# Kernel tuning notes

Measured on AMD Instinct MI355X. Metric: run time of the kernel, lower is better.

## Reference

```python
import jax, jax.numpy as jnp
import numpy as np


def setup_inputs() -> dict:
    key = jax.random.key(0)
    ks = jax.random.split(key, 8)
    T, D = 8192, 36
    return {
        "embeddings": jax.random.normal(ks[0], (T, D), dtype=jnp.float32),
        "WQ_prog": jax.random.normal(ks[1], (2, D), dtype=jnp.float32),
        "WK_prog": jax.random.normal(ks[2], (2, D), dtype=jnp.float32),
        "WV_op": jax.random.normal(ks[3], (1, D), dtype=jnp.float32),
        "WV_arg": jax.random.normal(ks[4], (1, D), dtype=jnp.float32),
        "WQ_stack": jax.random.normal(ks[5], (2, D), dtype=jnp.float32),
        "WK_stack": jax.random.normal(ks[6], (2, D), dtype=jnp.float32),
        "WV_stack": jax.random.normal(ks[7], (1, D), dtype=jnp.float32),
    }


def reference(embeddings, WQ_prog, WK_prog, WV_op, WV_arg, WQ_stack, WK_stack, WV_stack):
    # --- program-fetch head: hard-argmax attention ---
    Q_prog = embeddings @ WQ_prog.T          # (T, 2)
    K_prog = embeddings @ WK_prog.T          # (T, 2)
    V_op = embeddings @ WV_op.T              # (T, 1)
    V_arg = embeddings @ WV_arg.T            # (T, 1)
    scores_prog = Q_prog @ K_prog.T          # (T, T)
    best_prog = jnp.argmax(scores_prog, axis=1)   # (T,)
    fetched_ops = V_op[best_prog, 0]
    fetched_args = V_arg[best_prog, 0]

    # --- stack-fetch head: hard-argmax attention ---
    Q_stack = embeddings @ WQ_stack.T        # (T, 2)
    K_stack = embeddings @ WK_stack.T        # (T, 2)
    V_stack = embeddings @ WV_stack.T        # (T, 1)
    scores_stack = Q_stack @ K_stack.T       # (T, T)
    best_stack = jnp.argmax(scores_stack, axis=1)
    fetched_vals = V_stack[best_stack, 0]

    return (fetched_ops, fetched_args, fetched_vals)
```

## Files before the change

kernel.cpp:

```cpp
#include <hip/hip_runtime.h>
#include <math.h>

#define T 8192
#define D 36
#define NCH 8
#define CHUNK (T / NCH)


__global__ __launch_bounds__(256) void proj_kernel(
    const float* __restrict__ E,
    const float* __restrict__ WQp, const float* __restrict__ WKp,
    const float* __restrict__ WVop, const float* __restrict__ WVarg,
    const float* __restrict__ WQs, const float* __restrict__ WKs,
    const float* __restrict__ WVs, float* __restrict__ ws) {
    int t = blockIdx.x * blockDim.x + threadIdx.x;
    if (t >= T) return;
    float e[D];
    const float4* Er = (const float4*)(E + t * D);
#pragma unroll
    for (int i = 0; i < D / 4; ++i) {
        float4 v = Er[i];
        e[4 * i + 0] = v.x; e[4 * i + 1] = v.y;
        e[4 * i + 2] = v.z; e[4 * i + 3] = v.w;
    }
    float qp0 = 0.f, qp1 = 0.f, kp0 = 0.f, kp1 = 0.f;
    float qs0 = 0.f, qs1 = 0.f, ks0 = 0.f, ks1 = 0.f;
    float vop = 0.f, varg = 0.f, vs = 0.f;
#pragma unroll
    for (int d = 0; d < D; ++d) {
        float ed = e[d];
        qp0 = fmaf(ed, WQp[d], qp0);
        qp1 = fmaf(ed, WQp[D + d], qp1);
        kp0 = fmaf(ed, WKp[d], kp0);
        kp1 = fmaf(ed, WKp[D + d], kp1);
        qs0 = fmaf(ed, WQs[d], qs0);
        qs1 = fmaf(ed, WQs[D + d], qs1);
        ks0 = fmaf(ed, WKs[d], ks0);
        ks1 = fmaf(ed, WKs[D + d], ks1);
        vop  = fmaf(ed, WVop[d], vop);
        varg = fmaf(ed, WVarg[d], varg);
        vs   = fmaf(ed, WVs[d], vs);
    }
    ws[t]          = qp0;
    ws[T + t]      = qp1;
    ws[2 * T + 2 * t]     = kp0;
    ws[2 * T + 2 * t + 1] = kp1;
    ws[4 * T + t]  = qs0;
    ws[5 * T + t]  = qs1;
    ws[6 * T + 2 * t]     = ks0;
    ws[6 * T + 2 * t + 1] = ks1;
    ws[8 * T + t]  = vop;
    ws[9 * T + t]  = varg;
    ws[10 * T + t] = vs;
}

__global__ __launch_bounds__(256) void argmax_kernel(
    const float* __restrict__ wsf, float* __restrict__ pv, int* __restrict__ pi) {
    const int head = blockIdx.z;
    const float* Q0 = wsf + (head ? 4 * T : 0);
    const float* Q1 = Q0 + T;
    const float2* K = (const float2*)(wsf + (head ? 6 * T : 2 * T));

    __shared__ float2 sk[CHUNK];
    const int j0 = blockIdx.y * CHUNK;
    for (int k = threadIdx.x; k < CHUNK; k += 256) sk[k] = K[j0 + k];
    __syncthreads();

    const int row = blockIdx.x * 256 + threadIdx.x;
    const float q0 = Q0[row], q1 = Q1[row];
    float best = -INFINITY;
    int bi = 0;
#pragma unroll 8
    for (int k = 0; k < CHUNK; ++k) {
        float2 kk = sk[k];
        float s = fmaf(q0, kk.x, q1 * kk.y);
        bool gt = s > best;
        best = gt ? s : best;
        bi   = gt ? k : bi;
    }
    const int prow = head * T + row;
    pv[prow * NCH + blockIdx.y] = best;
    pi[prow * NCH + blockIdx.y] = j0 + bi;
}

__global__ __launch_bounds__(256) void finalize_kernel(
    const float* __restrict__ wsf, const float* __restrict__ pv,
    const int* __restrict__ pi, float* __restrict__ out) {
    int idx = blockIdx.x * blockDim.x + threadIdx.x;
    if (idx >= 2 * T) return;
    const int head = idx >> 13;
    const int row  = idx & (T - 1);
    float best = -INFINITY;
    int bi = 0;
#pragma unroll
    for (int c = 0; c < NCH; ++c) {
        float v = pv[idx * NCH + c];
        int   i2 = pi[idx * NCH + c];
        bool gt = v > best;
        best = gt ? v : best;
        bi   = gt ? i2 : bi;
    }
    const float* Vop  = wsf + 8 * T;
    const float* Varg = wsf + 9 * T;
    const float* Vs   = wsf + 10 * T;
    if (head == 0) {
        out[row]     = Vop[bi];
        out[T + row] = Varg[bi];
    } else {
        out[2 * T + row] = Vs[bi];
    }
}

extern "C" void kernel_launch(void* const* d_in, const int* in_sizes, int n_in,
                              void* d_out, int out_size, void* d_ws, size_t ws_size,
                              hipStream_t stream) {
    const float* E     = (const float*)d_in[0];
    const float* WQp   = (const float*)d_in[1];
    const float* WKp   = (const float*)d_in[2];
    const float* WVop  = (const float*)d_in[3];
    const float* WVarg = (const float*)d_in[4];
    const float* WQs   = (const float*)d_in[5];
    const float* WKs   = (const float*)d_in[6];
    const float* WVs   = (const float*)d_in[7];
    float* out = (float*)d_out;

    float* wsf = (float*)d_ws;
    float* pv  = wsf + 11 * T;
    int*   pi  = (int*)(wsf + 11 * T + 2 * T * NCH);

    proj_kernel<<<T / 256, 256, 0, stream>>>(E, WQp, WKp, WVop, WVarg, WQs, WKs, WVs, wsf);

    dim3 gB(T / 256, NCH, 2);
    argmax_kernel<<<gB, 256, 0, stream>>>(wsf, pv, pi);

    finalize_kernel<<<(2 * T) / 256, 256, 0, stream>>>(wsf, pv, pi, out);
}
```

Before: 100.1 us.

## Register-block argmax rows per thread and pack partial results as float2

Each argmax thread now handles four query rows, so every shared-memory key load is reused across four dot products. Keys are split into 64 chunks instead of 8, which gives a grid of 1024 blocks. Partial (value, index) pairs are packed into one float2 in a chunk-major layout, so finalize reads are coalesced. Q and K projections are stored as float2. The cost is that finalize must reduce 64 partials per row and the partial buffer grows eightfold.

```diff
diff --git a/kernel.cpp b/kernel.cpp
--- a/kernel.cpp
+++ b/kernel.cpp
@@ -3,8 +3,9 @@
 
 #define T 8192
 #define D 36
-#define NCH 8
+#define NCH 64
 #define CHUNK (T / NCH)
+#define RPT 4
 
 
 __global__ __launch_bounds__(256) void proj_kernel(
@@ -41,73 +42,83 @@
         varg = fmaf(ed, WVarg[d], varg);
         vs   = fmaf(ed, WVs[d], vs);
     }
-    ws[t]          = qp0;
-    ws[T + t]      = qp1;
-    ws[2 * T + 2 * t]     = kp0;
-    ws[2 * T + 2 * t + 1] = kp1;
-    ws[4 * T + t]  = qs0;
-    ws[5 * T + t]  = qs1;
-    ws[6 * T + 2 * t]     = ks0;
-    ws[6 * T + 2 * t + 1] = ks1;
+    float2* Qp = (float2*)ws;
+    float2* Kp = (float2*)(ws + 2 * T);
+    float2* Qs = (float2*)(ws + 4 * T);
+    float2* Ks = (float2*)(ws + 6 * T);
+    Qp[t] = make_float2(qp0, qp1);
+    Kp[t] = make_float2(kp0, kp1);
+    Qs[t] = make_float2(qs0, qs1);
+    Ks[t] = make_float2(ks0, ks1);
     ws[8 * T + t]  = vop;
     ws[9 * T + t]  = varg;
     ws[10 * T + t] = vs;
 }
 
 __global__ __launch_bounds__(256) void argmax_kernel(
-    const float* __restrict__ wsf, float* __restrict__ pv, int* __restrict__ pi) {
+    const float* __restrict__ wsf, float2* __restrict__ part) {
     const int head = blockIdx.z;
-    const float* Q0 = wsf + (head ? 4 * T : 0);
-    const float* Q1 = Q0 + T;
-    const float2* K = (const float2*)(wsf + (head ? 6 * T : 2 * T));
+    const float2* Q = (const float2*)(wsf + head * 4 * T);
+    const float2* K = (const float2*)(wsf + 2 * T + head * 4 * T);
 
     __shared__ float2 sk[CHUNK];
-    const int j0 = blockIdx.y * CHUNK;
-    for (int k = threadIdx.x; k < CHUNK; k += 256) sk[k] = K[j0 + k];
+    const int c  = blockIdx.y;
+    const int j0 = c * CHUNK;
+    if (threadIdx.x < CHUNK) sk[threadIdx.x] = K[j0 + threadIdx.x];
     __syncthreads();
 
-    const int row = blockIdx.x * 256 + threadIdx.x;
-    const float q0 = Q0[row], q1 = Q1[row];
-    float best = -INFINITY;
-    int bi = 0;
+    const int rbase = blockIdx.x * (256 * RPT) + threadIdx.x;
+    float2 q[RPT];
+    float best[RPT];
+    int   bi[RPT];
+#pragma unroll
+    for (int i = 0; i < RPT; ++i) {
+        q[i] = Q[rbase + 256 * i];
+        best[i] = -INFINITY;
+        bi[i] = 0;
+    }
 #pragma unroll 8
     for (int k = 0; k < CHUNK; ++k) {
         float2 kk = sk[k];
-        float s = fmaf(q0, kk.x, q1 * kk.y);
-        bool gt = s > best;
-        best = gt ? s : best;
-        bi   = gt ? k : bi;
+#pragma unroll
+        for (int i = 0; i < RPT; ++i) {
+            float s = fmaf(q[i].x, kk.x, q[i].y * kk.y);
+            bool gt = s > best[i];
+            best[i] = gt ? s : best[i];
+            bi[i]   = gt ? k : bi[i];
+        }
     }
-    const int prow = head * T + row;
-    pv[prow * NCH + blockIdx.y] = best;
-    pi[prow * NCH + blockIdx.y] = j0 + bi;
+#pragma unroll
+    for (int i = 0; i < RPT; ++i) {
+        const int prow = head * T + rbase + 256 * i;
+        part[c * (2 * T) + prow] = make_float2(best[i], __int_as_float(j0 + bi[i]));
+    }
 }
 
 __global__ __launch_bounds__(256) void finalize_kernel(
-    const float* __restrict__ wsf, const float* __restrict__ pv,
-    const int* __restrict__ pi, float* __restrict__ out) {
+    const float* __restrict__ wsf, const float2* __restrict__ part,
+    float* __restrict__ out) {
     int idx = blockIdx.x * blockDim.x + threadIdx.x;
     if (idx >= 2 * T) return;
+    float best = -INFINITY;
+    int bj = 0;
+#pragma unroll
+    for (int c = 0; c < NCH; ++c) {
+        float2 p = part[c * (2 * T) + idx];
+        bool gt = p.x > best;
+        best = gt ? p.x : best;
+        bj   = gt ? __float_as_int(p.y) : bj;
+    }
     const int head = idx >> 13;
     const int row  = idx & (T - 1);
-    float best = -INFINITY;
-    int bi = 0;
-#pragma unroll
-    for (int c = 0; c < NCH; ++c) {
-        float v = pv[idx * NCH + c];
-        int   i2 = pi[idx * NCH + c];
-        bool gt = v > best;
-        best = gt ? v : best;
-        bi   = gt ? i2 : bi;
-    }
     const float* Vop  = wsf + 8 * T;
     const float* Varg = wsf + 9 * T;
     const float* Vs   = wsf + 10 * T;
     if (head == 0) {
-        out[row]     = Vop[bi];
-        out[T + row] = Varg[bi];
+        out[row]     = Vop[bj];
+        out[T + row] = Varg[bj];
     } else {
-        out[2 * T + row] = Vs[bi];
+        out[2 * T + row] = Vs[bj];
     }
 }
 
@@ -125,13 +136,12 @@
     float* out = (float*)d_out;
 
     float* wsf = (float*)d_ws;
-    float* pv  = wsf + 11 * T;
-    int*   pi  = (int*)(wsf + 11 * T + 2 * T * NCH);
+    float2* part = (float2*)(wsf + 11 * T);
 
     proj_kernel<<<T / 256, 256, 0, stream>>>(E, WQp, WKp, WVop, WVarg, WQs, WKs, WVs, wsf);
 
-    dim3 gB(T / 256, NCH, 2);
-    argmax_kernel<<<gB, 256, 0, stream>>>(wsf, pv, pi);
+    dim3 gB(T / (256 * RPT), NCH, 2);
+    argmax_kernel<<<gB, 256, 0, stream>>>(wsf, part);
 
-    finalize_kernel<<<(2 * T) / 256, 256, 0, stream>>>(wsf, pv, pi, out);
+    finalize_kernel<<<(2 * T) / 256, 256, 0, stream>>>(wsf, part, out);
 }
```

Result: slower. 110.8 us (+10.7%).
